# Performance work log

Measured on AMD Instinct MI355X. Metric: run time of the kernel, lower is better.

Reference implementation:

```python
import jax, jax.numpy as jnp
import numpy as np

VOCAB = 540
EMBED = 128   # embedding_dim, also the LSTM 'batch' dim after the faithful .view reshape
HID = 100     # hidden_size == input_size == n_visits V (forced by the code)


def setup_inputs() -> dict:
    key = jax.random.key(0)
    ks = jax.random.split(key, 9)
    B, V, C = 256, 100, 40
    diag_x = jax.random.randint(ks[0], (B, V, C), 0, VOCAB, dtype=jnp.int64)
    mask = (jax.random.uniform(ks[1], (B, V, C)) < 0.85).astype(jnp.float32)
    s_e = 1.0 / np.sqrt(EMBED)
    s_h = 1.0 / np.sqrt(HID)
    return {
        "diag_x": diag_x,
        "mask": mask,
        "embed_table": jax.random.normal(ks[2], (VOCAB, EMBED), jnp.float32),
        "W_ih": jax.random.uniform(ks[3], (4 * HID, HID), jnp.float32, -s_h, s_h),
        "W_hh": jax.random.uniform(ks[4], (4 * HID, HID), jnp.float32, -s_h, s_h),
        "b_ih": jax.random.uniform(ks[5], (4 * HID,), jnp.float32, -s_h, s_h),
        "b_hh": jax.random.uniform(ks[6], (4 * HID,), jnp.float32, -s_h, s_h),
        "fc_w": jax.random.uniform(ks[7], (1, EMBED), jnp.float32, -s_e, s_e),
        "fc_b": jax.random.uniform(ks[8], (1,), jnp.float32, -s_e, s_e),
    }


def _forward(diag_x, mask, embed_table, W_ih, W_hh, b_ih, b_hh, fc_w, fc_b):
    B, V, C = diag_x.shape
    # masked embedding sum over codes-per-visit: [B,V,C,E] -> [B,V,E]
    emb = embed_table[diag_x] * mask[..., None]
    sum_embed = jnp.sum(emb, axis=2)
    # faithful to torch .view(B, 128, -1): a RESHAPE (not transpose) mixing V and E
    x_seq = sum_embed.reshape(B, EMBED, V)   # LSTM: time=B, batch=EMBED, feat=V(=HID)

    h0 = jnp.zeros((EMBED, HID), x_seq.dtype)
    c0 = jnp.zeros((EMBED, HID), x_seq.dtype)

    def step(carry, x_t):
        h, c = carry
        gates = x_t @ W_ih.T + b_ih + h @ W_hh.T + b_hh   # [EMBED, 4*HID]
        i, f, g, o = jnp.split(gates, 4, axis=-1)          # torch gate order i,f,g,o
        i = jax.nn.sigmoid(i); f = jax.nn.sigmoid(f)
        g = jnp.tanh(g);       o = jax.nn.sigmoid(o)
        c = f * c + i * g
        h = o * jnp.tanh(c)
        return (h, c), h

    _, hs = jax.lax.scan(step, (h0, c0), x_seq)            # [B, EMBED, HID]

    # get_last_visit: per-row max index of visits with any unmasked code (segment-max)
    has_visit = jnp.sum(mask, axis=-1) > 0                 # [B, V]
    last = jnp.max(jnp.where(has_visit, jnp.arange(V), -1), axis=1)  # [B]
    true_h = jnp.take_along_axis(hs, last[:, None, None], axis=2)[:, :, 0]  # [B, EMBED]

    out = jax.nn.sigmoid(true_h @ fc_w.T + fc_b)           # [B, 1]
    return out.reshape(-1)


def reference(diag_x, mask, embed_table, W_ih, W_hh, b_ih, b_hh, fc_w, fc_b):
    return _forward(diag_x, mask, embed_table, W_ih, W_hh, b_ih, b_hh, fc_w, fc_b)
```

## Files before the change

### kernel.cpp

```cpp
#include <hip/hip_runtime.h>
#include <math.h>

#define NB 256
#define NV 100
#define NC 40
#define NE 128
#define NH 100
#define NG 400

#define OFF_PRE   0
#define N_PRE     (NB*NE*NG)
#define OFF_TRUH  (OFF_PRE + N_PRE)
#define N_TRUH    (NB*NE)
#define OFF_LAST  (OFF_TRUH + N_TRUH)

__global__ __launch_bounds__(512, 2) void k_embgemm(
    const int* __restrict__ diag, const float* __restrict__ mask,
    const float* __restrict__ table, const float* __restrict__ Wih,
    const float* __restrict__ bih, const float* __restrict__ bhh,
    float* __restrict__ pre, int* __restrict__ last) {
  __shared__ __align__(16) float As[100][132];
  __shared__ __align__(16) float Bs[100][264];
  __shared__ __align__(16) float bias_s[256];
  __shared__ int lastred[4];

  const int tid = threadIdx.x;
  const int t   = blockIdx.x;
  const int e   = tid & 127;
  const int sub = tid >> 7;

  int vmax = -1;
  for (int i = 0; i < 25; ++i) {
    int fl = i * 512 + tid;
    int v  = fl >> 7;
    const float4* mrow4 = (const float4*)(mask + (t * NV + v) * NC);
    const int4*   drow4 = (const int4*)(diag + (t * NV + v) * NC);
    float acc = 0.f, msum = 0.f;
    #pragma unroll
    for (int cc = 0; cc < 10; ++cc) {
      float4 mm = mrow4[cc];
      int4   ii = drow4[cc];
      acc = fmaf(mm.x, table[ii.x * NE + e], acc); msum += mm.x;
      acc = fmaf(mm.y, table[ii.y * NE + e], acc); msum += mm.y;
      acc = fmaf(mm.z, table[ii.z * NE + e], acc); msum += mm.z;
      acc = fmaf(mm.w, table[ii.w * NE + e], acc); msum += mm.w;
    }
    int m = fl / 100, k = fl - m * 100;
    As[k][m] = acc;
    if (e == 0 && msum > 0.f) vmax = max(vmax, v);
  }
  if (e == 0) lastred[sub] = vmax;
  __syncthreads();
  if (tid == 0) {
    int l = max(max(lastred[0], lastred[1]), max(lastred[2], lastred[3]));
    last[t] = max(l, 0);
  }

  const int tm = tid & 15, tn = tid >> 4;
  for (int n0 = 0; n0 < NG; n0 += 256) {
    for (int idx = tid; idx < 25600; idx += 512) {
      int n = idx / 100, k = idx - n * 100;
      int jc = n0 + n;
      Bs[k][n] = (jc < NG) ? Wih[jc * 100 + k] : 0.f;
    }
    if (tid < 256) {
      int jc = n0 + tid;
      bias_s[tid] = (jc < NG) ? (bih[jc] + bhh[jc]) : 0.f;
    }
    __syncthreads();

    float acc[8][8] = {};
    #define PG_ROW(R, AX)                                                 \
      acc[R][0] = fmaf(AX, b0.x, acc[R][0]);                              \
      acc[R][1] = fmaf(AX, b0.y, acc[R][1]);                              \
      acc[R][2] = fmaf(AX, b0.z, acc[R][2]);                              \
      acc[R][3] = fmaf(AX, b0.w, acc[R][3]);                              \
      acc[R][4] = fmaf(AX, b1.x, acc[R][4]);                              \
      acc[R][5] = fmaf(AX, b1.y, acc[R][5]);                              \
      acc[R][6] = fmaf(AX, b1.z, acc[R][6]);                              \
      acc[R][7] = fmaf(AX, b1.w, acc[R][7]);
    for (int k = 0; k < 100; ++k) {
      float4 a0 = *(const float4*)&As[k][tm * 4];
      float4 a1 = *(const float4*)&As[k][64 + tm * 4];
      float4 b0 = *(const float4*)&Bs[k][tn * 4];
      float4 b1 = *(const float4*)&Bs[k][128 + tn * 4];
      PG_ROW(0, a0.x) PG_ROW(1, a0.y) PG_ROW(2, a0.z) PG_ROW(3, a0.w)
      PG_ROW(4, a1.x) PG_ROW(5, a1.y) PG_ROW(6, a1.z) PG_ROW(7, a1.w)
    }
    #undef PG_ROW

    const int c0 = n0 + tn * 4;
    const int c1 = n0 + 128 + tn * 4;
    float4 bv0 = *(const float4*)&bias_s[tn * 4];
    float4 bv1 = *(const float4*)&bias_s[128 + tn * 4];
    #pragma unroll
    for (int r = 0; r < 8; ++r) {
      int m = t * 128 + ((r < 4) ? (tm * 4 + r) : (64 + tm * 4 + (r - 4)));
      if (c0 < NG) {
        float4 st;
        st.x = acc[r][0] + bv0.x; st.y = acc[r][1] + bv0.y;
        st.z = acc[r][2] + bv0.z; st.w = acc[r][3] + bv0.w;
        *(float4*)&pre[m * NG + c0] = st;
      }
      if (c1 < NG) {
        float4 st;
        st.x = acc[r][4] + bv1.x; st.y = acc[r][5] + bv1.y;
        st.z = acc[r][6] + bv1.z; st.w = acc[r][7] + bv1.w;
        *(float4*)&pre[m * NG + c1] = st;
      }
    }
    __syncthreads();
  }
}

__device__ __forceinline__ float fast_sigmoid(float x) {
  return 1.f / (1.f + __expf(-x));
}
__device__ __forceinline__ float fast_tanh(float x) {
  float ax = fabsf(x);
  float e  = __expf(-2.f * ax);
  float t  = (1.f - e) / (1.f + e);
  return x < 0.f ? -t : t;
}

#define FMA4(A, W, H)                                                     \
  A = fmaf((H).x, (W).x, A); A = fmaf((H).y, (W).y, A);                   \
  A = fmaf((H).z, (W).z, A); A = fmaf((H).w, (W).w, A)

__global__ __launch_bounds__(512, 2) void k_lstm(
    const float* __restrict__ pre, const float* __restrict__ Whh,
    const int* __restrict__ last, float* __restrict__ truh) {
  __shared__ __align__(16) float h_s[100];
  __shared__ float g_s[NG];
  __shared__ int   last_s[NB];
  const int e = blockIdx.x;
  const int j = threadIdx.x;

  float4 w00, w01, w02, w03, w04, w05, w06, w07, w08, w09, w10, w11, w12,
         w13, w14, w15, w16, w17, w18, w19, w20, w21, w22, w23, w24;
  if (j < NG) {
    const float4* wr = (const float4*)(Whh + j * 100);
    w00 = wr[0];  w01 = wr[1];  w02 = wr[2];  w03 = wr[3];  w04 = wr[4];
    w05 = wr[5];  w06 = wr[6];  w07 = wr[7];  w08 = wr[8];  w09 = wr[9];
    w10 = wr[10]; w11 = wr[11]; w12 = wr[12]; w13 = wr[13]; w14 = wr[14];
    w15 = wr[15]; w16 = wr[16]; w17 = wr[17]; w18 = wr[18]; w19 = wr[19];
    w20 = wr[20]; w21 = wr[21]; w22 = wr[22]; w23 = wr[23]; w24 = wr[24];
  }
  if (j < NH) h_s[j] = 0.f;
  if (j < NB) last_s[j] = last[j];
  float c = 0.f;

  const float* pbase = pre + e * NG + j;
  float p0 = (j < NG) ? pbase[0]         : 0.f;
  float p1 = (j < NG) ? pbase[51200]     : 0.f;
  float p2 = (j < NG) ? pbase[2 * 51200] : 0.f;
  __syncthreads();

  for (int t = 0; t < NB; ++t) {
    float p3 = (j < NG && t + 3 < NB) ? pbase[(t + 3) * 51200] : 0.f;

    if (j < NG) {
      float a0 = p0, a1 = 0.f, a2 = 0.f, a3 = 0.f;
      const float4* h4 = (const float4*)h_s;
      float4 h;
      h = h4[0];  FMA4(a0, w00, h);
      h = h4[1];  FMA4(a1, w01, h);
      h = h4[2];  FMA4(a2, w02, h);
      h = h4[3];  FMA4(a3, w03, h);
      h = h4[4];  FMA4(a0, w04, h);
      h = h4[5];  FMA4(a1, w05, h);
      h = h4[6];  FMA4(a2, w06, h);
      h = h4[7];  FMA4(a3, w07, h);
      h = h4[8];  FMA4(a0, w08, h);
      h = h4[9];  FMA4(a1, w09, h);
      h = h4[10]; FMA4(a2, w10, h);
      h = h4[11]; FMA4(a3, w11, h);
      h = h4[12]; FMA4(a0, w12, h);
      h = h4[13]; FMA4(a1, w13, h);
      h = h4[14]; FMA4(a2, w14, h);
      h = h4[15]; FMA4(a3, w15, h);
      h = h4[16]; FMA4(a0, w16, h);
      h = h4[17]; FMA4(a1, w17, h);
      h = h4[18]; FMA4(a2, w18, h);
      h = h4[19]; FMA4(a3, w19, h);
      h = h4[20]; FMA4(a0, w20, h);
      h = h4[21]; FMA4(a1, w21, h);
      h = h4[22]; FMA4(a2, w22, h);
      h = h4[23]; FMA4(a3, w23, h);
      h = h4[24]; FMA4(a0, w24, h);
      float acc = (a0 + a1) + (a2 + a3);
      float act = (j >= 200 && j < 300) ? fast_tanh(acc) : fast_sigmoid(acc);
      g_s[j] = act;
    }
    __syncthreads();

    if (j < NH) {
      float ig = g_s[j], fg = g_s[100 + j], gg = g_s[200 + j], og = g_s[300 + j];
      c = fmaf(fg, c, ig * gg);
      float h = og * fast_tanh(c);
      h_s[j] = h;
      if (j == last_s[t]) truh[t * NE + e] = h;
    }
    __syncthreads();

    p0 = p1; p1 = p2; p2 = p3;
  }
}

__global__ __launch_bounds__(128) void k_fc(
    const float* __restrict__ truh, const float* __restrict__ fcw,
    const float* __restrict__ fcb, float* __restrict__ out) {
  int b = blockIdx.x, t = threadIdx.x;
  float v = truh[b * NE + t] * fcw[t];
  #pragma unroll
  for (int o = 32; o > 0; o >>= 1) v += __shfl_down(v, o);
  __shared__ float s[2];
  if ((t & 63) == 0) s[t >> 6] = v;
  __syncthreads();
  if (t == 0) {
    float sum = s[0] + s[1] + fcb[0];
    out[b] = 1.f / (1.f + __expf(-sum));
  }
}

extern "C" void kernel_launch(void* const* d_in, const int* in_sizes, int n_in,
                              void* d_out, int out_size, void* d_ws, size_t ws_size,
                              hipStream_t stream) {
  (void)in_sizes; (void)n_in; (void)out_size; (void)ws_size;
  const int*   diag  = (const int*)d_in[0];
  const float* mask  = (const float*)d_in[1];
  const float* table = (const float*)d_in[2];
  const float* Wih   = (const float*)d_in[3];
  const float* Whh   = (const float*)d_in[4];
  const float* bih   = (const float*)d_in[5];
  const float* bhh   = (const float*)d_in[6];
  const float* fcw   = (const float*)d_in[7];
  const float* fcb   = (const float*)d_in[8];

  float* ws   = (float*)d_ws;
  float* pre  = ws + OFF_PRE;
  float* truh = ws + OFF_TRUH;
  int*   last = (int*)(ws + OFF_LAST);
  float* out  = (float*)d_out;

  k_embgemm<<<dim3(NB),  dim3(512), 0, stream>>>(
      diag, mask, table, Wih, bih, bhh, pre, last);
  k_lstm   <<<dim3(NE),  dim3(512), 0, stream>>>(pre, Whh, last, truh);
  k_fc     <<<dim3(NB),  dim3(128), 0, stream>>>(truh, fcw, fcb, out);
}
```

Before: 378.3 us.

## Stream W_ih from global in one pass instead of LDS-staged two-pass tiles

The input-projection GEMM no longer transposes W_ih into a shared-memory tile. Each thread now reads float4 slices of W_ih directly from global memory (cache-resident) and accumulates all 400 gate columns in a single pass, using four 8x4 accumulator sets. This removes the strided LDS staging, the extra barriers and the padded second tile that did wasted work on zero columns, and it shrinks the kernel's shared-memory footprint. In exchange it needs about 128 live accumulators per thread under launch_bounds(512,2), which risks register spills, and every thread re-reads W_ih from cache.

```diff
diff --git a/kernel.cpp b/kernel.cpp
--- a/kernel.cpp
+++ b/kernel.cpp
@@ -20,8 +20,6 @@
     const float* __restrict__ bih, const float* __restrict__ bhh,
     float* __restrict__ pre, int* __restrict__ last) {
   __shared__ __align__(16) float As[100][132];
-  __shared__ __align__(16) float Bs[100][264];
-  __shared__ __align__(16) float bias_s[256];
   __shared__ int lastred[4];
 
   const int tid = threadIdx.x;
@@ -57,59 +55,80 @@
   }
 
   const int tm = tid & 15, tn = tid >> 4;
-  for (int n0 = 0; n0 < NG; n0 += 256) {
-    for (int idx = tid; idx < 25600; idx += 512) {
-      int n = idx / 100, k = idx - n * 100;
-      int jc = n0 + n;
-      Bs[k][n] = (jc < NG) ? Wih[jc * 100 + k] : 0.f;
-    }
-    if (tid < 256) {
-      int jc = n0 + tid;
-      bias_s[tid] = (jc < NG) ? (bih[jc] + bhh[jc]) : 0.f;
-    }
-    __syncthreads();
-
-    float acc[8][8] = {};
-    #define PG_ROW(R, AX)                                                 \
-      acc[R][0] = fmaf(AX, b0.x, acc[R][0]);                              \
-      acc[R][1] = fmaf(AX, b0.y, acc[R][1]);                              \
-      acc[R][2] = fmaf(AX, b0.z, acc[R][2]);                              \
-      acc[R][3] = fmaf(AX, b0.w, acc[R][3]);                              \
-      acc[R][4] = fmaf(AX, b1.x, acc[R][4]);                              \
-      acc[R][5] = fmaf(AX, b1.y, acc[R][5]);                              \
-      acc[R][6] = fmaf(AX, b1.z, acc[R][6]);                              \
-      acc[R][7] = fmaf(AX, b1.w, acc[R][7]);
-    for (int k = 0; k < 100; ++k) {
-      float4 a0 = *(const float4*)&As[k][tm * 4];
-      float4 a1 = *(const float4*)&As[k][64 + tm * 4];
-      float4 b0 = *(const float4*)&Bs[k][tn * 4];
-      float4 b1 = *(const float4*)&Bs[k][128 + tn * 4];
-      PG_ROW(0, a0.x) PG_ROW(1, a0.y) PG_ROW(2, a0.z) PG_ROW(3, a0.w)
-      PG_ROW(4, a1.x) PG_ROW(5, a1.y) PG_ROW(6, a1.z) PG_ROW(7, a1.w)
-    }
-    #undef PG_ROW
-
-    const int c0 = n0 + tn * 4;
-    const int c1 = n0 + 128 + tn * 4;
-    float4 bv0 = *(const float4*)&bias_s[tn * 4];
-    float4 bv1 = *(const float4*)&bias_s[128 + tn * 4];
-    #pragma unroll
-    for (int r = 0; r < 8; ++r) {
-      int m = t * 128 + ((r < 4) ? (tm * 4 + r) : (64 + tm * 4 + (r - 4)));
-      if (c0 < NG) {
-        float4 st;
-        st.x = acc[r][0] + bv0.x; st.y = acc[r][1] + bv0.y;
-        st.z = acc[r][2] + bv0.z; st.w = acc[r][3] + bv0.w;
-        *(float4*)&pre[m * NG + c0] = st;
-      }
-      if (c1 < NG) {
-        float4 st;
-        st.x = acc[r][4] + bv1.x; st.y = acc[r][5] + bv1.y;
-        st.z = acc[r][6] + bv1.z; st.w = acc[r][7] + bv1.w;
-        *(float4*)&pre[m * NG + c1] = st;
-      }
-    }
-    __syncthreads();
+  const int j0 = tn * 4, j1 = 128 + j0, j2 = 256 + j0, j3 = 384 + j0;
+  const bool has3 = (tn < 4);
+  float acc0[8][4] = {}, acc1[8][4] = {}, acc2[8][4] = {}, acc3[8][4] = {};
+  float4 bA[4], bB[4];
+
+  #define ROWUPD(ACC, AX, B, COMP, R)                                     \
+    ACC[R][0] = fmaf(AX, B[0].COMP, ACC[R][0]);                           \
+    ACC[R][1] = fmaf(AX, B[1].COMP, ACC[R][1]);                           \
+    ACC[R][2] = fmaf(AX, B[2].COMP, ACC[R][2]);                           \
+    ACC[R][3] = fmaf(AX, B[3].COMP, ACC[R][3]);
+  #define GRP8(ACC, B, COMP)                                              \
+    ROWUPD(ACC, a0.x, B, COMP, 0) ROWUPD(ACC, a0.y, B, COMP, 1)           \
+    ROWUPD(ACC, a0.z, B, COMP, 2) ROWUPD(ACC, a0.w, B, COMP, 3)           \
+    ROWUPD(ACC, a1.x, B, COMP, 4) ROWUPD(ACC, a1.y, B, COMP, 5)           \
+    ROWUPD(ACC, a1.z, B, COMP, 6) ROWUPD(ACC, a1.w, B, COMP, 7)
+  #define KSTEP2(KOFF, COMP, ACCX, ACCY, GUARDY)                          \
+    { float4 a0 = *(const float4*)&As[k4 + KOFF][tm * 4];                 \
+      float4 a1 = *(const float4*)&As[k4 + KOFF][64 + tm * 4];            \
+      GRP8(ACCX, bA, COMP)                                                \
+      if (GUARDY) { GRP8(ACCY, bB, COMP) } }
+
+  for (int k4 = 0; k4 < 100; k4 += 4) {
+    #pragma unroll
+    for (int c = 0; c < 4; ++c) {
+      bA[c] = *(const float4*)&Wih[(j0 + c) * 100 + k4];
+      bB[c] = *(const float4*)&Wih[(j1 + c) * 100 + k4];
+    }
+    KSTEP2(0, x, acc0, acc1, true) KSTEP2(1, y, acc0, acc1, true)
+    KSTEP2(2, z, acc0, acc1, true) KSTEP2(3, w, acc0, acc1, true)
+    #pragma unroll
+    for (int c = 0; c < 4; ++c)
+      bA[c] = *(const float4*)&Wih[(j2 + c) * 100 + k4];
+    if (has3) {
+      #pragma unroll
+      for (int c = 0; c < 4; ++c)
+        bB[c] = *(const float4*)&Wih[(j3 + c) * 100 + k4];
+    }
+    KSTEP2(0, x, acc2, acc3, has3) KSTEP2(1, y, acc2, acc3, has3)
+    KSTEP2(2, z, acc2, acc3, has3) KSTEP2(3, w, acc2, acc3, has3)
+  }
+  #undef KSTEP2
+  #undef GRP8
+  #undef ROWUPD
+
+  float bv0[4], bv1[4], bv2[4], bv3[4] = {};
+  #pragma unroll
+  for (int c = 0; c < 4; ++c) {
+    bv0[c] = bih[j0 + c] + bhh[j0 + c];
+    bv1[c] = bih[j1 + c] + bhh[j1 + c];
+    bv2[c] = bih[j2 + c] + bhh[j2 + c];
+  }
+  if (has3) {
+    #pragma unroll
+    for (int c = 0; c < 4; ++c) bv3[c] = bih[j3 + c] + bhh[j3 + c];
+  }
+  #pragma unroll
+  for (int r = 0; r < 8; ++r) {
+    int m = t * 128 + ((r < 4) ? (tm * 4 + r) : (64 + tm * 4 + (r - 4)));
+    float* prow = pre + m * NG;
+    float4 s;
+    s.x = acc0[r][0] + bv0[0]; s.y = acc0[r][1] + bv0[1];
+    s.z = acc0[r][2] + bv0[2]; s.w = acc0[r][3] + bv0[3];
+    *(float4*)&prow[j0] = s;
+    s.x = acc1[r][0] + bv1[0]; s.y = acc1[r][1] + bv1[1];
+    s.z = acc1[r][2] + bv1[2]; s.w = acc1[r][3] + bv1[3];
+    *(float4*)&prow[j1] = s;
+    s.x = acc2[r][0] + bv2[0]; s.y = acc2[r][1] + bv2[1];
+    s.z = acc2[r][2] + bv2[2]; s.w = acc2[r][3] + bv2[3];
+    *(float4*)&prow[j2] = s;
+    if (has3) {
+      s.x = acc3[r][0] + bv3[0]; s.y = acc3[r][1] + bv3[1];
+      s.z = acc3[r][2] + bv3[2]; s.w = acc3[r][3] + bv3[3];
+      *(float4*)&prow[j3] = s;
+    }
   }
 }
 
```

New measurement: 424.2 us. 12.1% more time.
